# Kernel tuning notes

Measured on AMD Instinct MI355X. Metric: run time of the kernel, lower is better.

Reference implementation:

```python
import jax, jax.numpy as jnp
import numpy as np

T, I, H, L = 2048, 64, 512, 5  # seq len, input feat, hidden, layers


def _lstm_layer(x_seq, w_ih, w_hh, b_ih, b_hh):
    """Single-layer LSTM over time, batch=1. x_seq: [T, in]. Returns [T, H]."""
    n_hidden = w_hh.shape[1]
    b = b_ih + b_hh  # fuse biases once

    def step(carry, x_t):
        h, c = carry
        gates = w_ih @ x_t + w_hh @ h + b  # [4H]
        i, f, g, o = jnp.split(gates, 4)
        i = jax.nn.sigmoid(i)
        f = jax.nn.sigmoid(f)
        g = jnp.tanh(g)
        o = jax.nn.sigmoid(o)
        c = f * c + i * g
        h = o * jnp.tanh(c)
        return (h, c), h

    h0 = jnp.zeros((n_hidden,), x_seq.dtype)
    (_, _), hs = jax.lax.scan(step, (h0, h0), x_seq)
    return hs


def setup_inputs() -> dict:
    key = jax.random.key(0)
    ks = jax.random.split(key, 12)
    s = 1.0 / np.sqrt(H)  # PyTorch-style U(-1/sqrt(H), 1/sqrt(H)) scale, approximated with scaled normal
    return {
        "x": jax.random.normal(ks[0], (T, I), jnp.float32),
        "w_ih0": jax.random.normal(ks[1], (4 * H, I), jnp.float32) * s,
        "w_hh0": jax.random.normal(ks[2], (4 * H, H), jnp.float32) * s,
        "b_ih0": jax.random.normal(ks[3], (4 * H,), jnp.float32) * s,
        "b_hh0": jax.random.normal(ks[4], (4 * H,), jnp.float32) * s,
        "w_ih": jax.random.normal(ks[5], (L - 1, 4 * H, H), jnp.float32) * s,
        "w_hh": jax.random.normal(ks[6], (L - 1, 4 * H, H), jnp.float32) * s,
        "b_ih": jax.random.normal(ks[7], (L - 1, 4 * H), jnp.float32) * s,
        "b_hh": jax.random.normal(ks[8], (L - 1, 4 * H), jnp.float32) * s,
        "w_lin": jax.random.normal(ks[9], (1, H), jnp.float32) * s,
        "b_lin": jax.random.normal(ks[10], (1,), jnp.float32) * s,
    }


def reference(x, w_ih0, w_hh0, b_ih0, b_hh0, w_ih, w_hh, b_ih, b_hh, w_lin, b_lin):
    # 5-layer LSTM (dropout=0 / inference), batch = 1
    h = _lstm_layer(x, w_ih0, w_hh0, b_ih0, b_hh0)  # [T, H]
    for l in range(w_ih.shape[0]):  # fixed small layer loop
        h = _lstm_layer(h, w_ih[l], w_hh[l], b_ih[l], b_hh[l])
    e = h @ w_lin.T + b_lin                # [T, 1]
    w = jax.nn.softmax(jnp.tanh(e), axis=0)  # softmax over time
    res = jnp.mean(h * w, axis=0, keepdims=True)  # [1, H] (matches torch (T,1,H)*(T,1) mean over axis 0)
    return res
```

## Files before the change

kernel.cpp:

```cpp
#include <hip/hip_runtime.h>
#include <math.h>

#define TT 2048
#define II 64
#define HH 512
#define LL 5
#define RING 64
#define BPL 32
#define NBLK (LL * BPL)
#define WPB 16
#define SPIN_LIMIT 2000000L

typedef unsigned long long u64;
typedef unsigned u32;

__device__ __forceinline__ float wave_sum(float v) {
#pragma unroll
  for (int m = 32; m > 0; m >>= 1) v += __shfl_xor(v, m, 64);
  return v;
}

__device__ __forceinline__ float wave_max(float v) {
#pragma unroll
  for (int m = 32; m > 0; m >>= 1) v = fmaxf(v, __shfl_xor(v, m, 64));
  return v;
}

__device__ __forceinline__ float sigmoidf_(float v) {
  return 1.0f / (1.0f + expf(-v));
}

__device__ __forceinline__ u32 ld4(const u32* p) {
  return __hip_atomic_load((u32*)p, __ATOMIC_RELAXED, __HIP_MEMORY_SCOPE_AGENT);
}
__device__ __forceinline__ void st4(u32* p, u32 v) {
  __hip_atomic_store(p, v, __ATOMIC_RELAXED, __HIP_MEMORY_SCOPE_AGENT);
}
__device__ __forceinline__ u64 ld8(const u64* p) {
  return __hip_atomic_load((u64*)p, __ATOMIC_RELAXED, __HIP_MEMORY_SCOPE_AGENT);
}
__device__ __forceinline__ void st8(u64* p, u64 v) {
  __hip_atomic_store(p, v, __ATOMIC_RELAXED, __HIP_MEMORY_SCOPE_AGENT);
}

__device__ __forceinline__ float poll_ring(const u64* p, u32 want) {
  u64 a = ld8(p);
  u64 b = ld8(p);
  long sp = 0;
  while ((u32)(a >> 32) != want) {
    a = b;
    b = ld8(p);
    if (++sp > SPIN_LIMIT) { a = ((u64)want << 32); break; }
  }
  return __uint_as_float((u32)a);
}

__device__ __forceinline__ void wait_ge(u32* p, u32 v) {
  long spins = 0;
  while (ld4(p) < v) {
    if (++spins > SPIN_LIMIT) {
      __hip_atomic_fetch_max(p, v, __ATOMIC_RELAXED, __HIP_MEMORY_SCOPE_AGENT);
      break;
    }
  }
}

__device__ __forceinline__ void grid_barrier(u32* arrive, u32* gen, u32 idx) {
  __syncthreads();
  if (threadIdx.x == 0) {
    __threadfence();
    u32 target = (u32)NBLK * (idx + 1u);
    u32 prev = __hip_atomic_fetch_add(arrive, 1u, __ATOMIC_RELAXED, __HIP_MEMORY_SCOPE_AGENT);
    if (prev + 1u == target) {
      __hip_atomic_store(gen, idx + 1u, __ATOMIC_RELAXED, __HIP_MEMORY_SCOPE_AGENT);
    } else {
      wait_ge(gen, idx + 1u);
    }
    __threadfence();
  }
  __syncthreads();
}

extern "C" __global__ void __launch_bounds__(1024)
__attribute__((amdgpu_waves_per_eu(4, 4)))
lstm_pipe(
    const float* __restrict__ x,
    const float* __restrict__ w_ih0, const float* __restrict__ w_hh0,
    const float* __restrict__ b_ih0, const float* __restrict__ b_hh0,
    const float* __restrict__ w_ih, const float* __restrict__ w_hh,
    const float* __restrict__ b_ih, const float* __restrict__ b_hh,
    const float* __restrict__ w_lin, const float* __restrict__ b_lin,
    float* __restrict__ out, float* __restrict__ ws) {
  extern __shared__ float wihs[];
  __shared__ float hbuf[HH];
  __shared__ float xbuf[HH];
  __shared__ float sbuf[20];

  u32* cnt = (u32*)ws;
  u32* garr = cnt + 320;
  u32* ggen = cnt + 336;

  u64* ring = (u64*)((char*)ws + 4096);
  float* h4 = (float*)(ring + (size_t)LL * RING * HH);
  float* h4T = h4 + (size_t)TT * HH;
  float* scores = h4T + (size_t)HH * TT;
  float* pbuf = scores + TT;
  float* red = pbuf + TT;

  const int b = blockIdx.x;
  const int tid = threadIdx.x;
  const int wv = tid >> 6;
  const int lane = tid & 63;
  const int layer = b / BPL;
  const int slot = b % BPL;
  const int j = slot * WPB + wv;
  const bool is_last = (layer == LL - 1);

  u32* prog_l = cnt + layer * 64;
  u32* prog_lp1 = cnt + (layer + 1) * 64;
  u64* myring = ring + (size_t)layer * RING * HH;
  u64* prevring = ring + (size_t)(layer > 0 ? layer - 1 : 0) * RING * HH;

  float whh[4][8], bias[4];
  {
    const float* WHH = (layer == 0) ? w_hh0 : (w_hh + (size_t)(layer - 1) * 4 * HH * HH);
#pragma unroll
    for (int g = 0; g < 4; ++g) {
      const int row = g * HH + j;
#pragma unroll
      for (int m = 0; m < 8; ++m) whh[g][m] = WHH[(size_t)row * HH + m * 64 + lane];
    }
    if (layer == 0) {
#pragma unroll
      for (int g = 0; g < 4; ++g) bias[g] = b_ih0[g * HH + j] + b_hh0[g * HH + j];
    } else {
      const float* BIH = b_ih + (size_t)(layer - 1) * 4 * HH;
      const float* BHH = b_hh + (size_t)(layer - 1) * 4 * HH;
#pragma unroll
      for (int g = 0; g < 4; ++g) bias[g] = BIH[g * HH + j] + BHH[g * HH + j];
    }
    const float* WIH = (layer == 0) ? (const float*)0
                                    : (w_ih + (size_t)(layer - 1) * 4 * HH * HH);
    for (int f = tid; f < WPB * 4 * HH; f += 1024) {
      const int jj = f >> 11;
      const int g = (f >> 9) & 3;
      const int k = f & 511;
      const int row = g * HH + slot * WPB + jj;
      float v;
      if (layer == 0) v = (k < II) ? w_ih0[(size_t)row * II + k] : 0.0f;
      else v = WIH[(size_t)row * HH + k];
      wihs[f] = v;
    }
#pragma unroll
    for (int g = 0; g < 4; ++g) {
#pragma unroll
      for (int m = 0; m < 8; ++m) asm volatile("" : "+v"(whh[g][m]));
      asm volatile("" : "+v"(bias[g]));
    }
  }
  __syncthreads();

  float c = 0.0f;

  for (int t = 0; t < TT; ++t) {
    const int sl = t & (RING - 1);
    if (tid < HH) {
      if (t > 0) {
        hbuf[tid] =
            poll_ring(myring + (size_t)((t - 1) & (RING - 1)) * HH + tid, (u32)t);
      } else {
        hbuf[tid] = 0.0f;
      }
      if (tid == 0) {
        if (slot == 0 && t > 0 && (t & 3) == 0) st4(prog_l, (u32)t);
        if (layer < LL - 1 && t >= 64 && (t & 7) == 0) {
          long sp = 0;
          while (ld4(prog_lp1) < (u32)(t - 40) && ++sp < SPIN_LIMIT) {}
        }
      }
    } else {
      const int k = tid - HH;
      if (layer == 0) {
        xbuf[k] = (k < II) ? x[(size_t)t * II + k] : 0.0f;
      } else {
        xbuf[k] = poll_ring(prevring + (size_t)sl * HH + k, (u32)(t + 1));
      }
    }
    __syncthreads();

    float hp[8], xin[8];
#pragma unroll
    for (int m = 0; m < 8; ++m) {
      hp[m] = hbuf[m * 64 + lane];
      xin[m] = xbuf[m * 64 + lane];
    }
    float ai = 0.0f, af = 0.0f, ag = 0.0f, ao = 0.0f;
#pragma unroll
    for (int m = 0; m < 8; ++m) {
      ai = fmaf(whh[0][m], hp[m], ai);
      af = fmaf(whh[1][m], hp[m], af);
      ag = fmaf(whh[2][m], hp[m], ag);
      ao = fmaf(whh[3][m], hp[m], ao);
    }
    const float* wb = wihs + (size_t)wv * 4 * HH;
#pragma unroll
    for (int m = 0; m < 8; ++m) {
      const int o = m * 64 + lane;
      ai = fmaf(wb[0 * HH + o], xin[m], ai);
      af = fmaf(wb[1 * HH + o], xin[m], af);
      ag = fmaf(wb[2 * HH + o], xin[m], ag);
      ao = fmaf(wb[3 * HH + o], xin[m], ao);
    }
    ai = wave_sum(ai); af = wave_sum(af); ag = wave_sum(ag); ao = wave_sum(ao);
    float gi = sigmoidf_(ai + bias[0]);
    float gf = sigmoidf_(af + bias[1]);
    float gg = tanhf(ag + bias[2]);
    float go = sigmoidf_(ao + bias[3]);
    c = gf * c + gi * gg;
    float h = go * tanhf(c);

    if (lane == 0) {
      st8(myring + (size_t)sl * HH + j,
          (((u64)(u32)(t + 1)) << 32) | (u64)__float_as_uint(h));
      if (is_last) {
        h4[(size_t)t * HH + j] = h;
        h4T[(size_t)j * TT + t] = h;
      }
    }
    __syncthreads();
  }

  grid_barrier(garr, ggen, 0u);

  {
    const int gw = b * WPB + wv;
    if (gw < TT) {
      const int t = gw;
      const float4* hp4 = (const float4*)(h4 + (size_t)t * HH + lane * 8);
      const float4* wl4 = (const float4*)(w_lin + lane * 8);
      float4 a = hp4[0], d = hp4[1], wa = wl4[0], wd = wl4[1];
      float acc = 0.0f;
      acc = fmaf(a.x, wa.x, acc); acc = fmaf(a.y, wa.y, acc);
      acc = fmaf(a.z, wa.z, acc); acc = fmaf(a.w, wa.w, acc);
      acc = fmaf(d.x, wd.x, acc); acc = fmaf(d.y, wd.y, acc);
      acc = fmaf(d.z, wd.z, acc); acc = fmaf(d.w, wd.w, acc);
      acc = wave_sum(acc);
      float sc = tanhf(acc + b_lin[0]);
      if (lane == 0) scores[t] = sc;
    }
  }
  grid_barrier(garr, ggen, 1u);

  if (b == 0) {
    float s0 = scores[tid];
    float s1 = scores[tid + 1024];
    float m = fmaxf(s0, s1);
    m = wave_max(m);
    if (lane == 0) sbuf[wv] = m;
    __syncthreads();
    if (tid == 0) {
      float M = sbuf[0];
      for (int k = 1; k < 16; ++k) M = fmaxf(M, sbuf[k]);
      sbuf[16] = M;
    }
    __syncthreads();
    float M = sbuf[16];
    float p0 = expf(s0 - M), p1 = expf(s1 - M);
    pbuf[tid] = p0;
    pbuf[tid + 1024] = p1;
    float ssum = wave_sum(p0 + p1);
    __syncthreads();
    if (lane == 0) sbuf[wv] = ssum;
    __syncthreads();
    if (tid == 0) {
      float S = 0.0f;
      for (int k = 0; k < 16; ++k) S += sbuf[k];
      red[0] = 1.0f / ((float)TT * S);
    }
  }
  grid_barrier(garr, ggen, 2u);

  {
    const int gw = b * WPB + wv;
    if (gw < HH) {
      const float scale = red[0];
      const float* hr = h4T + (size_t)gw * TT + lane * 32;
      const float* pr = pbuf + lane * 32;
      float acc = 0.0f;
#pragma unroll
      for (int m = 0; m < 32; ++m) acc = fmaf(hr[m], pr[m], acc);
      acc = wave_sum(acc);
      if (lane == 0) out[gw] = scale * acc;
    }
  }
}

extern "C" void kernel_launch(void* const* d_in, const int* in_sizes, int n_in,
                              void* d_out, int out_size, void* d_ws, size_t ws_size,
                              hipStream_t stream) {
  hipFuncSetAttribute((const void*)lstm_pipe,
                      hipFuncAttributeMaxDynamicSharedMemorySize, 131072);
  hipMemsetAsync(d_ws, 0, 4096, stream);
  lstm_pipe<<<dim3(NBLK), dim3(1024), 131072, stream>>>(
      (const float*)d_in[0],
      (const float*)d_in[1], (const float*)d_in[2],
      (const float*)d_in[3], (const float*)d_in[4],
      (const float*)d_in[5], (const float*)d_in[6],
      (const float*)d_in[7], (const float*)d_in[8],
      (const float*)d_in[9], (const float*)d_in[10],
      (float*)d_out, (float*)d_ws);
}
```

Measured before the change: 7.515 ms.

## Map each LSTM layer's blocks onto one XCD via XCC_ID claiming

Launches 256 blocks and has each block read its hardware XCC ID, then atomically claim a slot within the layer matching that XCD. All 32 blocks of a layer then share one chiplet's L2, which is meant to cut the cross-XCD latency of the ring polling between blocks of the same layer. If the claims come out unbalanced, it falls back to the old block-index mapping. This adds two extra grid barriers and idle surplus blocks, and assumes all 256 blocks are co-resident.

```diff
diff --git a/kernel.cpp b/kernel.cpp
--- a/kernel.cpp
+++ b/kernel.cpp
@@ -7,9 +7,10 @@
 #define LL 5
 #define RING 64
 #define BPL 32
-#define NBLK (LL * BPL)
+#define NBLK 256
 #define WPB 16
 #define SPIN_LIMIT 2000000L
+#define BARRIER_SPIN 20000000L
 
 typedef unsigned long long u64;
 typedef unsigned u32;
@@ -58,7 +59,7 @@
 __device__ __forceinline__ void wait_ge(u32* p, u32 v) {
   long spins = 0;
   while (ld4(p) < v) {
-    if (++spins > SPIN_LIMIT) {
+    if (++spins > BARRIER_SPIN) {
       __hip_atomic_fetch_max(p, v, __ATOMIC_RELAXED, __HIP_MEMORY_SCOPE_AGENT);
       break;
     }
@@ -95,10 +96,13 @@
   __shared__ float hbuf[HH];
   __shared__ float xbuf[HH];
   __shared__ float sbuf[20];
+  __shared__ int s_layer, s_slot;
 
   u32* cnt = (u32*)ws;
   u32* garr = cnt + 320;
   u32* ggen = cnt + 336;
+  u32* claims = cnt + 352;
+  u32* flagp = cnt + 448;
 
   u64* ring = (u64*)((char*)ws + 4096);
   float* h4 = (float*)(ring + (size_t)LL * RING * HH);
@@ -111,126 +115,153 @@
   const int tid = threadIdx.x;
   const int wv = tid >> 6;
   const int lane = tid & 63;
-  const int layer = b / BPL;
-  const int slot = b % BPL;
-  const int j = slot * WPB + wv;
-  const bool is_last = (layer == LL - 1);
-
-  u32* prog_l = cnt + layer * 64;
-  u32* prog_lp1 = cnt + (layer + 1) * 64;
-  u64* myring = ring + (size_t)layer * RING * HH;
-  u64* prevring = ring + (size_t)(layer > 0 ? layer - 1 : 0) * RING * HH;
-
-  float whh[4][8], bias[4];
-  {
-    const float* WHH = (layer == 0) ? w_hh0 : (w_hh + (size_t)(layer - 1) * 4 * HH * HH);
-#pragma unroll
-    for (int g = 0; g < 4; ++g) {
-      const int row = g * HH + j;
-#pragma unroll
-      for (int m = 0; m < 8; ++m) whh[g][m] = WHH[(size_t)row * HH + m * 64 + lane];
-    }
-    if (layer == 0) {
-#pragma unroll
-      for (int g = 0; g < 4; ++g) bias[g] = b_ih0[g * HH + j] + b_hh0[g * HH + j];
-    } else {
-      const float* BIH = b_ih + (size_t)(layer - 1) * 4 * HH;
-      const float* BHH = b_hh + (size_t)(layer - 1) * 4 * HH;
-#pragma unroll
-      for (int g = 0; g < 4; ++g) bias[g] = BIH[g * HH + j] + BHH[g * HH + j];
-    }
-    const float* WIH = (layer == 0) ? (const float*)0
-                                    : (w_ih + (size_t)(layer - 1) * 4 * HH * HH);
-    for (int f = tid; f < WPB * 4 * HH; f += 1024) {
-      const int jj = f >> 11;
-      const int g = (f >> 9) & 3;
-      const int k = f & 511;
-      const int row = g * HH + slot * WPB + jj;
-      float v;
-      if (layer == 0) v = (k < II) ? w_ih0[(size_t)row * II + k] : 0.0f;
-      else v = WIH[(size_t)row * HH + k];
-      wihs[f] = v;
-    }
-#pragma unroll
-    for (int g = 0; g < 4; ++g) {
-#pragma unroll
-      for (int m = 0; m < 8; ++m) asm volatile("" : "+v"(whh[g][m]));
-      asm volatile("" : "+v"(bias[g]));
-    }
+
+  if (tid == 0) {
+    u32 xcc = 0;
+    asm volatile("s_getreg_b32 %0, hwreg(HW_REG_XCC_ID)" : "=s"(xcc));
+    xcc &= 7u;
+    int layer = -1, slot = 0;
+    if (xcc < LL) {
+      u32 idx = __hip_atomic_fetch_add(claims + xcc * 16, 1u, __ATOMIC_RELAXED,
+                                       __HIP_MEMORY_SCOPE_AGENT);
+      if (idx < (u32)BPL) { layer = (int)xcc; slot = (int)idx; }
+    }
+    s_layer = layer; s_slot = slot;
+  }
+  grid_barrier(garr, ggen, 0u);
+  if (b == 0 && tid == 0) {
+    bool ok = true;
+    for (int l = 0; l < LL; ++l) ok &= (ld4(claims + l * 16) >= (u32)BPL);
+    st4(flagp, ok ? 1u : 2u);
+  }
+  grid_barrier(garr, ggen, 1u);
+  if (tid == 0 && ld4(flagp) == 2u) {
+    s_layer = (b < LL * BPL) ? (b / BPL) : -1;
+    s_slot = (b < LL * BPL) ? (b % BPL) : 0;
   }
   __syncthreads();
-
-  float c = 0.0f;
-
-  for (int t = 0; t < TT; ++t) {
-    const int sl = t & (RING - 1);
-    if (tid < HH) {
-      if (t > 0) {
-        hbuf[tid] =
-            poll_ring(myring + (size_t)((t - 1) & (RING - 1)) * HH + tid, (u32)t);
+  const int layer = s_layer;
+  const int slot = s_slot;
+
+  if (layer >= 0) {
+    const int j = slot * WPB + wv;
+    const bool is_last = (layer == LL - 1);
+    u32* prog_l = cnt + layer * 64;
+    u32* prog_lp1 = cnt + (layer + 1) * 64;
+    u64* myring = ring + (size_t)layer * RING * HH;
+    u64* prevring = ring + (size_t)(layer > 0 ? layer - 1 : 0) * RING * HH;
+
+    float whh[4][8], bias[4];
+    {
+      const float* WHH = (layer == 0) ? w_hh0 : (w_hh + (size_t)(layer - 1) * 4 * HH * HH);
+#pragma unroll
+      for (int g = 0; g < 4; ++g) {
+        const int row = g * HH + j;
+#pragma unroll
+        for (int m = 0; m < 8; ++m) whh[g][m] = WHH[(size_t)row * HH + m * 64 + lane];
+      }
+      if (layer == 0) {
+#pragma unroll
+        for (int g = 0; g < 4; ++g) bias[g] = b_ih0[g * HH + j] + b_hh0[g * HH + j];
       } else {
-        hbuf[tid] = 0.0f;
-      }
-      if (tid == 0) {
-        if (slot == 0 && t > 0 && (t & 3) == 0) st4(prog_l, (u32)t);
-        if (layer < LL - 1 && t >= 64 && (t & 7) == 0) {
-          long sp = 0;
-          while (ld4(prog_lp1) < (u32)(t - 40) && ++sp < SPIN_LIMIT) {}
+        const float* BIH = b_ih + (size_t)(layer - 1) * 4 * HH;
+        const float* BHH = b_hh + (size_t)(layer - 1) * 4 * HH;
+#pragma unroll
+        for (int g = 0; g < 4; ++g) bias[g] = BIH[g * HH + j] + BHH[g * HH + j];
+      }
+      const float* WIH = (layer == 0) ? (const float*)0
+                                      : (w_ih + (size_t)(layer - 1) * 4 * HH * HH);
+      for (int f = tid; f < WPB * 4 * HH; f += 1024) {
+        const int jj = f >> 11;
+        const int g = (f >> 9) & 3;
+        const int k = f & 511;
+        const int row = g * HH + slot * WPB + jj;
+        float v;
+        if (layer == 0) v = (k < II) ? w_ih0[(size_t)row * II + k] : 0.0f;
+        else v = WIH[(size_t)row * HH + k];
+        wihs[f] = v;
+      }
+#pragma unroll
+      for (int g = 0; g < 4; ++g) {
+#pragma unroll
+        for (int m = 0; m < 8; ++m) asm volatile("" : "+v"(whh[g][m]));
+        asm volatile("" : "+v"(bias[g]));
+      }
+    }
+    __syncthreads();
+
+    float c = 0.0f;
+
+    for (int t = 0; t < TT; ++t) {
+      const int sl = t & (RING - 1);
+      if (tid < HH) {
+        if (t > 0) {
+          hbuf[tid] =
+              poll_ring(myring + (size_t)((t - 1) & (RING - 1)) * HH + tid, (u32)t);
+        } else {
+          hbuf[tid] = 0.0f;
         }
-      }
-    } else {
-      const int k = tid - HH;
-      if (layer == 0) {
-        xbuf[k] = (k < II) ? x[(size_t)t * II + k] : 0.0f;
+        if (tid == 0) {
+          if (slot == 0 && t > 0 && (t & 3) == 0) st4(prog_l, (u32)t);
+          if (layer < LL - 1 && t >= 64 && (t & 7) == 0) {
+            long sp = 0;
+            while (ld4(prog_lp1) < (u32)(t - 40) && ++sp < SPIN_LIMIT) {}
+          }
+        }
       } else {
-        xbuf[k] = poll_ring(prevring + (size_t)sl * HH + k, (u32)(t + 1));
-      }
-    }
-    __syncthreads();
-
-    float hp[8], xin[8];
-#pragma unroll
-    for (int m = 0; m < 8; ++m) {
-      hp[m] = hbuf[m * 64 + lane];
-      xin[m] = xbuf[m * 64 + lane];
-    }
-    float ai = 0.0f, af = 0.0f, ag = 0.0f, ao = 0.0f;
-#pragma unroll
-    for (int m = 0; m < 8; ++m) {
-      ai = fmaf(whh[0][m], hp[m], ai);
-      af = fmaf(whh[1][m], hp[m], af);
-      ag = fmaf(whh[2][m], hp[m], ag);
-      ao = fmaf(whh[3][m], hp[m], ao);
-    }
-    const float* wb = wihs + (size_t)wv * 4 * HH;
-#pragma unroll
-    for (int m = 0; m < 8; ++m) {
-      const int o = m * 64 + lane;
-      ai = fmaf(wb[0 * HH + o], xin[m], ai);
-      af = fmaf(wb[1 * HH + o], xin[m], af);
-      ag = fmaf(wb[2 * HH + o], xin[m], ag);
-      ao = fmaf(wb[3 * HH + o], xin[m], ao);
-    }
-    ai = wave_sum(ai); af = wave_sum(af); ag = wave_sum(ag); ao = wave_sum(ao);
-    float gi = sigmoidf_(ai + bias[0]);
-    float gf = sigmoidf_(af + bias[1]);
-    float gg = tanhf(ag + bias[2]);
-    float go = sigmoidf_(ao + bias[3]);
-    c = gf * c + gi * gg;
-    float h = go * tanhf(c);
-
-    if (lane == 0) {
-      st8(myring + (size_t)sl * HH + j,
-          (((u64)(u32)(t + 1)) << 32) | (u64)__float_as_uint(h));
-      if (is_last) {
-        h4[(size_t)t * HH + j] = h;
-        h4T[(size_t)j * TT + t] = h;
-      }
-    }
-    __syncthreads();
-  }
-
-  grid_barrier(garr, ggen, 0u);
+        const int k = tid - HH;
+        if (layer == 0) {
+          xbuf[k] = (k < II) ? x[(size_t)t * II + k] : 0.0f;
+        } else {
+          xbuf[k] = poll_ring(prevring + (size_t)sl * HH + k, (u32)(t + 1));
+        }
+      }
+      __syncthreads();
+
+      float hp[8], xin[8];
+#pragma unroll
+      for (int m = 0; m < 8; ++m) {
+        hp[m] = hbuf[m * 64 + lane];
+        xin[m] = xbuf[m * 64 + lane];
+      }
+      float ai = 0.0f, af = 0.0f, ag = 0.0f, ao = 0.0f;
+#pragma unroll
+      for (int m = 0; m < 8; ++m) {
+        ai = fmaf(whh[0][m], hp[m], ai);
+        af = fmaf(whh[1][m], hp[m], af);
+        ag = fmaf(whh[2][m], hp[m], ag);
+        ao = fmaf(whh[3][m], hp[m], ao);
+      }
+      const float* wb = wihs + (size_t)wv * 4 * HH;
+#pragma unroll
+      for (int m = 0; m < 8; ++m) {
+        const int o = m * 64 + lane;
+        ai = fmaf(wb[0 * HH + o], xin[m], ai);
+        af = fmaf(wb[1 * HH + o], xin[m], af);
+        ag = fmaf(wb[2 * HH + o], xin[m], ag);
+        ao = fmaf(wb[3 * HH + o], xin[m], ao);
+      }
+      ai = wave_sum(ai); af = wave_sum(af); ag = wave_sum(ag); ao = wave_sum(ao);
+      float gi = sigmoidf_(ai + bias[0]);
+      float gf = sigmoidf_(af + bias[1]);
+      float gg = tanhf(ag + bias[2]);
+      float go = sigmoidf_(ao + bias[3]);
+      c = gf * c + gi * gg;
+      float h = go * tanhf(c);
+
+      if (lane == 0) {
+        st8(myring + (size_t)sl * HH + j,
+            (((u64)(u32)(t + 1)) << 32) | (u64)__float_as_uint(h));
+        if (is_last) {
+          h4[(size_t)t * HH + j] = h;
+          h4T[(size_t)j * TT + t] = h;
+        }
+      }
+      __syncthreads();
+    }
+  }
+
+  grid_barrier(garr, ggen, 2u);
 
   {
     const int gw = b * WPB + wv;
@@ -249,7 +280,7 @@
       if (lane == 0) scores[t] = sc;
     }
   }
-  grid_barrier(garr, ggen, 1u);
+  grid_barrier(garr, ggen, 3u);
 
   if (b == 0) {
     float s0 = scores[tid];
@@ -278,7 +309,7 @@
       red[0] = 1.0f / ((float)TT * S);
     }
   }
-  grid_barrier(garr, ggen, 2u);
+  grid_barrier(garr, ggen, 4u);
 
   {
     const int gw = b * WPB + wv;
```

After: 7.465 ms. About the same (-0.7%).
